# Kernel tuning notes

Measured on AMD Instinct MI355X. Metric: run time of the kernel, lower is better.

Reference implementation:

```python
import jax, jax.numpy as jnp
import numpy as np

B, N_MAX, H, STEPS = 8, 36, 64, 5


def setup_inputs() -> dict:
    key = jax.random.key(0)
    ks = jax.random.split(key, 6)
    bound = 1.0 / np.sqrt(H)
    return {
        "edge_wgt": jax.random.normal(ks[0], (B, N_MAX, N_MAX, H, H), dtype=jnp.float32) * 0.1,
        "nodes_embed": jax.random.normal(ks[1], (B, N_MAX, H), dtype=jnp.float32),
        "mask": jnp.ones((B, N_MAX, 1), dtype=jnp.float32),
        "w_ih": jax.random.uniform(ks[2], (3 * H, H), jnp.float32, -bound, bound),
        "w_hh": jax.random.uniform(ks[3], (3 * H, H), jnp.float32, -bound, bound),
        "b_ih": jax.random.uniform(ks[4], (3 * H,), jnp.float32, -bound, bound),
        "b_hh": jax.random.uniform(ks[5], (3 * H,), jnp.float32, -bound, bound),
    }


def _gru_cell(x, h, w_ih, w_hh, b_ih, b_hh):
    # torch.nn.GRUCell math; x, h: [..., H]
    gi = x @ w_ih.T + b_ih
    gh = h @ w_hh.T + b_hh
    i_r, i_z, i_n = jnp.split(gi, 3, axis=-1)
    h_r, h_z, h_n = jnp.split(gh, 3, axis=-1)
    r = jax.nn.sigmoid(i_r + h_r)
    z = jax.nn.sigmoid(i_z + h_z)
    n = jnp.tanh(i_n + r * h_n)
    return (1.0 - z) * n + z * h


def reference(edge_wgt, nodes_embed, mask, w_ih, w_hh, b_ih, b_hh):
    n_max = edge_wgt.shape[1]
    inv_n2 = 1.0 / (n_max * n_max)
    nodes = nodes_embed
    for _ in range(STEPS):
        # messages[b,j,k] = (1/n^2) * sum_{i,l} edge_wgt[b,i,j,k,l] * nodes[b,i,l]
        messages = jnp.einsum('bijkl,bil->bjk', edge_wgt, nodes) * inv_n2
        nodes = _gru_cell(messages, nodes, w_ih, w_hh, b_ih, b_hh) * mask
    return nodes
```

## Files before the change

kernel.cpp:

```cpp
#include <hip/hip_runtime.h>
#include <hip/hip_bf16.h>


#define BB 8
#define NN 36
#define HH 64
#define GG 12
#define IPG (NN / GG)
#define NSTEPS 5

__device__ __forceinline__ unsigned bf16rtn(float f) {
    unsigned u = __float_as_uint(f);
    return (u + 0x7FFFu + ((u >> 16) & 1u)) >> 16;
}

__global__ __launch_bounds__(64) void einsum_f32_cvt(
    const float* __restrict__ edge,
    const float* __restrict__ nodes,
    float* __restrict__ partial,
    uint2* __restrict__ ebf)
{
    const int lane = threadIdx.x;
    const int bid  = blockIdx.x;
    const int g = bid % GG;
    const int j = (bid / GG) % NN;
    const int b = bid / (GG * NN);

    const int l4 = lane & 15;

    float acc[16];
    #pragma unroll
    for (int it = 0; it < 16; ++it) acc[it] = 0.f;

    #pragma unroll
    for (int ii = 0; ii < IPG; ++ii) {
        const int i = g * IPG + ii;
        const float4 v = *(const float4*)(nodes + (b * NN + i) * HH + l4 * 4);
        const size_t blkElem = (size_t)((b * NN + i) * NN + j) * (HH * HH);
        const float4* __restrict__ Wb = (const float4*)(edge + blkElem);
        uint2* __restrict__ Eb = ebf + (blkElem >> 2);
        #pragma unroll
        for (int it = 0; it < 16; ++it) {
            const float4 w = Wb[it * 64 + lane];
            acc[it] = fmaf(w.x, v.x, acc[it]);
            acc[it] = fmaf(w.y, v.y, acc[it]);
            acc[it] = fmaf(w.z, v.z, acc[it]);
            acc[it] = fmaf(w.w, v.w, acc[it]);
            uint2 pk;
            pk.x = bf16rtn(w.x) | (bf16rtn(w.y) << 16);
            pk.y = bf16rtn(w.z) | (bf16rtn(w.w) << 16);
            Eb[it * 64 + lane] = pk;
        }
    }

    #pragma unroll
    for (int m = 1; m < 16; m <<= 1) {
        #pragma unroll
        for (int it = 0; it < 16; ++it)
            acc[it] += __shfl_xor(acc[it], m, 64);
    }

    const int p  = lane & 15;
    const int gq = lane >> 4;
    float outv = acc[0];
    #pragma unroll
    for (int t = 1; t < 16; ++t) outv = (p == t) ? acc[t] : outv;

    partial[(size_t)bid * HH + (4 * p + gq)] = outv;
}

__global__ __launch_bounds__(64) void einsum_bf16(
    const uint4* __restrict__ ebf,
    const float* __restrict__ nodes,
    float* __restrict__ partial)
{
    const int lane = threadIdx.x;
    const int bid  = blockIdx.x;
    const int g = bid % GG;
    const int j = (bid / GG) % NN;
    const int b = bid / (GG * NN);

    const int l8 = lane & 7;

    float acc[8];
    #pragma unroll
    for (int it = 0; it < 8; ++it) acc[it] = 0.f;

    #pragma unroll
    for (int ii = 0; ii < IPG; ++ii) {
        const int i = g * IPG + ii;
        const float* np_ = nodes + (b * NN + i) * HH + l8 * 8;
        const float4 v0 = *(const float4*)(np_);
        const float4 v1 = *(const float4*)(np_ + 4);
        const size_t blkElem = (size_t)((b * NN + i) * NN + j) * (HH * HH);
        const uint4* __restrict__ Wb = ebf + (blkElem >> 3);
        #pragma unroll
        for (int it = 0; it < 8; ++it) {
            const uint4 w = Wb[it * 64 + lane];
            acc[it] = fmaf(__uint_as_float(w.x << 16),          v0.x, acc[it]);
            acc[it] = fmaf(__uint_as_float(w.x & 0xffff0000u),  v0.y, acc[it]);
            acc[it] = fmaf(__uint_as_float(w.y << 16),          v0.z, acc[it]);
            acc[it] = fmaf(__uint_as_float(w.y & 0xffff0000u),  v0.w, acc[it]);
            acc[it] = fmaf(__uint_as_float(w.z << 16),          v1.x, acc[it]);
            acc[it] = fmaf(__uint_as_float(w.z & 0xffff0000u),  v1.y, acc[it]);
            acc[it] = fmaf(__uint_as_float(w.w << 16),          v1.z, acc[it]);
            acc[it] = fmaf(__uint_as_float(w.w & 0xffff0000u),  v1.w, acc[it]);
        }
    }

    #pragma unroll
    for (int m = 1; m < 8; m <<= 1) {
        #pragma unroll
        for (int it = 0; it < 8; ++it)
            acc[it] += __shfl_xor(acc[it], m, 64);
    }

    const int p  = lane & 7;
    const int gq = lane >> 3;
    float outv = acc[0];
    #pragma unroll
    for (int t = 1; t < 8; ++t) outv = (p == t) ? acc[t] : outv;

    partial[(size_t)bid * HH + (8 * p + gq)] = outv;
}

__global__ __launch_bounds__(64) void gru_step(
    const float* __restrict__ partial,
    const float* __restrict__ nodes_in,
    const float* __restrict__ mask,
    const float* __restrict__ w_ih,
    const float* __restrict__ w_hh,
    const float* __restrict__ b_ih,
    const float* __restrict__ b_hh,
    float* __restrict__ nodes_out)
{
    const int t  = threadIdx.x;
    const int bj = blockIdx.x;
    const float inv_n2 = 1.0f / (float)(NN * NN);

    float m = 0.f;
    #pragma unroll
    for (int g = 0; g < GG; ++g)
        m += partial[((size_t)bj * GG + g) * HH + t];
    m *= inv_n2;
    const float h = nodes_in[bj * HH + t];

    __shared__ float ms[HH];
    __shared__ float hs[HH];
    ms[t] = m;
    hs[t] = h;
    __syncthreads();

    float gi0 = b_ih[t], gi1 = b_ih[HH + t], gi2 = b_ih[2 * HH + t];
    float gh0 = b_hh[t], gh1 = b_hh[HH + t], gh2 = b_hh[2 * HH + t];

    const float4* __restrict__ wi0 = (const float4*)(w_ih + (0 * HH + t) * HH);
    const float4* __restrict__ wi1 = (const float4*)(w_ih + (1 * HH + t) * HH);
    const float4* __restrict__ wi2 = (const float4*)(w_ih + (2 * HH + t) * HH);
    const float4* __restrict__ wh0 = (const float4*)(w_hh + (0 * HH + t) * HH);
    const float4* __restrict__ wh1 = (const float4*)(w_hh + (1 * HH + t) * HH);
    const float4* __restrict__ wh2 = (const float4*)(w_hh + (2 * HH + t) * HH);

    #pragma unroll
    for (int k4 = 0; k4 < HH / 4; ++k4) {
        const float4 mv = *(const float4*)&ms[k4 * 4];
        const float4 hv = *(const float4*)&hs[k4 * 4];
        float4 a;
        a = wi0[k4]; gi0 += a.x * mv.x + a.y * mv.y + a.z * mv.z + a.w * mv.w;
        a = wi1[k4]; gi1 += a.x * mv.x + a.y * mv.y + a.z * mv.z + a.w * mv.w;
        a = wi2[k4]; gi2 += a.x * mv.x + a.y * mv.y + a.z * mv.z + a.w * mv.w;
        a = wh0[k4]; gh0 += a.x * hv.x + a.y * hv.y + a.z * hv.z + a.w * hv.w;
        a = wh1[k4]; gh1 += a.x * hv.x + a.y * hv.y + a.z * hv.z + a.w * hv.w;
        a = wh2[k4]; gh2 += a.x * hv.x + a.y * hv.y + a.z * hv.z + a.w * hv.w;
    }

    const float r = 1.f / (1.f + expf(-(gi0 + gh0)));
    const float z = 1.f / (1.f + expf(-(gi1 + gh1)));
    const float n = tanhf(gi2 + r * gh2);
    float outv = (1.f - z) * n + z * h;
    outv *= mask[bj];
    nodes_out[bj * HH + t] = outv;
}

extern "C" void kernel_launch(void* const* d_in, const int* in_sizes, int n_in,
                              void* d_out, int out_size, void* d_ws, size_t ws_size,
                              hipStream_t stream) {
    const float* edge   = (const float*)d_in[0];
    const float* nodes0 = (const float*)d_in[1];
    const float* mask   = (const float*)d_in[2];
    const float* w_ih   = (const float*)d_in[3];
    const float* w_hh   = (const float*)d_in[4];
    const float* b_ih   = (const float*)d_in[5];
    const float* b_hh   = (const float*)d_in[6];
    float* out = (float*)d_out;

    float* ws = (float*)d_ws;
    const int nodes_elems = BB * NN * HH;
    float* nodesA  = ws;
    float* nodesB  = ws + nodes_elems;
    float* partial = ws + 2 * nodes_elems;
    float* ebf_f   = partial + (size_t)BB * NN * GG * HH;
    uint2* ebf2 = (uint2*)ebf_f;
    const uint4* ebf4 = (const uint4*)ebf_f;

    const int grid_e = BB * NN * GG;

    const float* cur = nodes0;
    for (int s = 0; s < NSTEPS; ++s) {
        if (s == 0)
            einsum_f32_cvt<<<grid_e, 64, 0, stream>>>(edge, cur, partial, ebf2);
        else
            einsum_bf16<<<grid_e, 64, 0, stream>>>(ebf4, cur, partial);
        float* nxt = (s == NSTEPS - 1) ? out : ((s & 1) ? nodesB : nodesA);
        gru_step<<<BB * NN, 64, 0, stream>>>(partial, cur, mask,
                                             w_ih, w_hh, b_ih, b_hh, nxt);
        cur = nxt;
    }
}
```

Measured before the change: 151.3 us.

## Fuse GRU update into the bf16 einsum kernel with redundant per-block recompute

The separate gru_step launch is folded into the start of each following bf16 einsum kernel. Each einsum block reduces the previous step's partial sums and runs the GRU cell for its own i-nodes in shared memory, then feeds those fresh nodes into the bf16 contraction. Partial buffers are double-buffered, and a final GRU-only kernel finishes the last step. This removes four kernel launches and the global round-trip of node states. The cost is that every node's GRU is recomputed redundantly by all 36 j-blocks, which adds weight loads and serial latency at the start of each block.

```diff
diff --git a/kernel.cpp b/kernel.cpp
--- a/kernel.cpp
+++ b/kernel.cpp
@@ -8,10 +8,44 @@
 #define GG 12
 #define IPG (NN / GG)
 #define NSTEPS 5
+#define INVN2 (1.0f / (float)(NN * NN))
 
 __device__ __forceinline__ unsigned bf16rtn(float f) {
     unsigned u = __float_as_uint(f);
     return (u + 0x7FFFu + ((u >> 16) & 1u)) >> 16;
+}
+
+__device__ __forceinline__ float gru_lane(
+    const float* __restrict__ ms, const float* __restrict__ hs, int t,
+    const float* __restrict__ w_ih, const float* __restrict__ w_hh,
+    const float* __restrict__ b_ih, const float* __restrict__ b_hh)
+{
+    float gi0 = b_ih[t], gi1 = b_ih[HH + t], gi2 = b_ih[2 * HH + t];
+    float gh0 = b_hh[t], gh1 = b_hh[HH + t], gh2 = b_hh[2 * HH + t];
+
+    const float4* __restrict__ wi0 = (const float4*)(w_ih + (0 * HH + t) * HH);
+    const float4* __restrict__ wi1 = (const float4*)(w_ih + (1 * HH + t) * HH);
+    const float4* __restrict__ wi2 = (const float4*)(w_ih + (2 * HH + t) * HH);
+    const float4* __restrict__ wh0 = (const float4*)(w_hh + (0 * HH + t) * HH);
+    const float4* __restrict__ wh1 = (const float4*)(w_hh + (1 * HH + t) * HH);
+    const float4* __restrict__ wh2 = (const float4*)(w_hh + (2 * HH + t) * HH);
+
+    #pragma unroll
+    for (int k4 = 0; k4 < HH / 4; ++k4) {
+        const float4 mv = *(const float4*)&ms[k4 * 4];
+        const float4 hv = *(const float4*)&hs[k4 * 4];
+        float4 a;
+        a = wi0[k4]; gi0 += a.x * mv.x + a.y * mv.y + a.z * mv.z + a.w * mv.w;
+        a = wi1[k4]; gi1 += a.x * mv.x + a.y * mv.y + a.z * mv.z + a.w * mv.w;
+        a = wi2[k4]; gi2 += a.x * mv.x + a.y * mv.y + a.z * mv.z + a.w * mv.w;
+        a = wh0[k4]; gh0 += a.x * hv.x + a.y * hv.y + a.z * hv.z + a.w * hv.w;
+        a = wh1[k4]; gh1 += a.x * hv.x + a.y * hv.y + a.z * hv.z + a.w * hv.w;
+        a = wh2[k4]; gh2 += a.x * hv.x + a.y * hv.y + a.z * hv.z + a.w * hv.w;
+    }
+    const float r = 1.f / (1.f + expf(-(gi0 + gh0)));
+    const float z = 1.f / (1.f + expf(-(gi1 + gh1)));
+    const float n = tanhf(gi2 + r * gh2);
+    return (1.f - z) * n + z * hs[t];
 }
 
 __global__ __launch_bounds__(64) void einsum_f32_cvt(
@@ -69,16 +103,50 @@
     partial[(size_t)bid * HH + (4 * p + gq)] = outv;
 }
 
-__global__ __launch_bounds__(64) void einsum_bf16(
+__global__ __launch_bounds__(64) void einsum_bf16_fused(
     const uint4* __restrict__ ebf,
-    const float* __restrict__ nodes,
-    float* __restrict__ partial)
+    const float* __restrict__ partial_prev,
+    const float* __restrict__ nodes_pp,
+    const float* __restrict__ mask,
+    const float* __restrict__ w_ih,
+    const float* __restrict__ w_hh,
+    const float* __restrict__ b_ih,
+    const float* __restrict__ b_hh,
+    float* __restrict__ nodes_out,
+    float* __restrict__ partial_out)
 {
     const int lane = threadIdx.x;
     const int bid  = blockIdx.x;
     const int g = bid % GG;
     const int j = (bid / GG) % NN;
     const int b = bid / (GG * NN);
+    const int t = lane;
+
+    __shared__ float ms[IPG][HH];
+    __shared__ float hs[IPG][HH];
+    __shared__ float nd[IPG][HH];
+
+    #pragma unroll
+    for (int ii = 0; ii < IPG; ++ii) {
+        const int i = g * IPG + ii;
+        float m = 0.f;
+        #pragma unroll
+        for (int gp = 0; gp < GG; ++gp)
+            m += partial_prev[((size_t)(b * NN + i) * GG + gp) * HH + t];
+        ms[ii][t] = m * INVN2;
+        hs[ii][t] = nodes_pp[(b * NN + i) * HH + t];
+    }
+    __syncthreads();
+
+    #pragma unroll
+    for (int ii = 0; ii < IPG; ++ii) {
+        const int i = g * IPG + ii;
+        float outv = gru_lane(ms[ii], hs[ii], t, w_ih, w_hh, b_ih, b_hh);
+        outv *= mask[b * NN + i];
+        nd[ii][t] = outv;
+        nodes_out[(b * NN + i) * HH + t] = outv;
+    }
+    __syncthreads();
 
     const int l8 = lane & 7;
 
@@ -89,9 +157,8 @@
     #pragma unroll
     for (int ii = 0; ii < IPG; ++ii) {
         const int i = g * IPG + ii;
-        const float* np_ = nodes + (b * NN + i) * HH + l8 * 8;
-        const float4 v0 = *(const float4*)(np_);
-        const float4 v1 = *(const float4*)(np_ + 4);
+        const float4 v0 = *(const float4*)&nd[ii][l8 * 8];
+        const float4 v1 = *(const float4*)&nd[ii][l8 * 8 + 4];
         const size_t blkElem = (size_t)((b * NN + i) * NN + j) * (HH * HH);
         const uint4* __restrict__ Wb = ebf + (blkElem >> 3);
         #pragma unroll
@@ -119,12 +186,12 @@
     const int gq = lane >> 3;
     float outv = acc[0];
     #pragma unroll
-    for (int t = 1; t < 8; ++t) outv = (p == t) ? acc[t] : outv;
-
-    partial[(size_t)bid * HH + (8 * p + gq)] = outv;
-}
-
-__global__ __launch_bounds__(64) void gru_step(
+    for (int tt = 1; tt < 8; ++tt) outv = (p == tt) ? acc[tt] : outv;
+
+    partial_out[(size_t)bid * HH + (8 * p + gq)] = outv;
+}
+
+__global__ __launch_bounds__(64) void gru_final(
     const float* __restrict__ partial,
     const float* __restrict__ nodes_in,
     const float* __restrict__ mask,
@@ -136,48 +203,19 @@
 {
     const int t  = threadIdx.x;
     const int bj = blockIdx.x;
-    const float inv_n2 = 1.0f / (float)(NN * NN);
 
     float m = 0.f;
     #pragma unroll
     for (int g = 0; g < GG; ++g)
         m += partial[((size_t)bj * GG + g) * HH + t];
-    m *= inv_n2;
-    const float h = nodes_in[bj * HH + t];
 
     __shared__ float ms[HH];
     __shared__ float hs[HH];
-    ms[t] = m;
-    hs[t] = h;
+    ms[t] = m * INVN2;
+    hs[t] = nodes_in[bj * HH + t];
     __syncthreads();
 
-    float gi0 = b_ih[t], gi1 = b_ih[HH + t], gi2 = b_ih[2 * HH + t];
-    float gh0 = b_hh[t], gh1 = b_hh[HH + t], gh2 = b_hh[2 * HH + t];
-
-    const float4* __restrict__ wi0 = (const float4*)(w_ih + (0 * HH + t) * HH);
-    const float4* __restrict__ wi1 = (const float4*)(w_ih + (1 * HH + t) * HH);
-    const float4* __restrict__ wi2 = (const float4*)(w_ih + (2 * HH + t) * HH);
-    const float4* __restrict__ wh0 = (const float4*)(w_hh + (0 * HH + t) * HH);
-    const float4* __restrict__ wh1 = (const float4*)(w_hh + (1 * HH + t) * HH);
-    const float4* __restrict__ wh2 = (const float4*)(w_hh + (2 * HH + t) * HH);
-
-    #pragma unroll
-    for (int k4 = 0; k4 < HH / 4; ++k4) {
-        const float4 mv = *(const float4*)&ms[k4 * 4];
-        const float4 hv = *(const float4*)&hs[k4 * 4];
-        float4 a;
-        a = wi0[k4]; gi0 += a.x * mv.x + a.y * mv.y + a.z * mv.z + a.w * mv.w;
-        a = wi1[k4]; gi1 += a.x * mv.x + a.y * mv.y + a.z * mv.z + a.w * mv.w;
-        a = wi2[k4]; gi2 += a.x * mv.x + a.y * mv.y + a.z * mv.z + a.w * mv.w;
-        a = wh0[k4]; gh0 += a.x * hv.x + a.y * hv.y + a.z * hv.z + a.w * hv.w;
-        a = wh1[k4]; gh1 += a.x * hv.x + a.y * hv.y + a.z * hv.z + a.w * hv.w;
-        a = wh2[k4]; gh2 += a.x * hv.x + a.y * hv.y + a.z * hv.z + a.w * hv.w;
-    }
-
-    const float r = 1.f / (1.f + expf(-(gi0 + gh0)));
-    const float z = 1.f / (1.f + expf(-(gi1 + gh1)));
-    const float n = tanhf(gi2 + r * gh2);
-    float outv = (1.f - z) * n + z * h;
+    float outv = gru_lane(ms, hs, t, w_ih, w_hh, b_ih, b_hh);
     outv *= mask[bj];
     nodes_out[bj * HH + t] = outv;
 }
@@ -195,25 +233,32 @@
     float* out = (float*)d_out;
 
     float* ws = (float*)d_ws;
-    const int nodes_elems = BB * NN * HH;
-    float* nodesA  = ws;
-    float* nodesB  = ws + nodes_elems;
-    float* partial = ws + 2 * nodes_elems;
-    float* ebf_f   = partial + (size_t)BB * NN * GG * HH;
+    const int nodes_elems   = BB * NN * HH;
+    const int partial_elems = BB * NN * GG * HH;
+    float* nodesA   = ws;
+    float* nodesB   = ws + nodes_elems;
+    float* partialA = ws + 2 * nodes_elems;
+    float* partialB = partialA + partial_elems;
+    float* ebf_f    = partialB + partial_elems;
     uint2* ebf2 = (uint2*)ebf_f;
     const uint4* ebf4 = (const uint4*)ebf_f;
 
     const int grid_e = BB * NN * GG;
 
-    const float* cur = nodes0;
-    for (int s = 0; s < NSTEPS; ++s) {
-        if (s == 0)
-            einsum_f32_cvt<<<grid_e, 64, 0, stream>>>(edge, cur, partial, ebf2);
-        else
-            einsum_bf16<<<grid_e, 64, 0, stream>>>(ebf4, cur, partial);
-        float* nxt = (s == NSTEPS - 1) ? out : ((s & 1) ? nodesB : nodesA);
-        gru_step<<<BB * NN, 64, 0, stream>>>(partial, cur, mask,
-                                             w_ih, w_hh, b_ih, b_hh, nxt);
-        cur = nxt;
-    }
-}
+    einsum_f32_cvt<<<grid_e, 64, 0, stream>>>(edge, nodes0, partialA, ebf2);
+
+    einsum_bf16_fused<<<grid_e, 64, 0, stream>>>(ebf4, partialA, nodes0, mask,
+                                                 w_ih, w_hh, b_ih, b_hh,
+                                                 nodesA, partialB);
+    einsum_bf16_fused<<<grid_e, 64, 0, stream>>>(ebf4, partialB, nodesA, mask,
+                                                 w_ih, w_hh, b_ih, b_hh,
+                                                 nodesB, partialA);
+    einsum_bf16_fused<<<grid_e, 64, 0, stream>>>(ebf4, partialA, nodesB, mask,
+                                                 w_ih, w_hh, b_ih, b_hh,
+                                                 nodesA, partialB);
+    einsum_bf16_fused<<<grid_e, 64, 0, stream>>>(ebf4, partialB, nodesA, mask,
+                                                 w_ih, w_hh, b_ih, b_hh,
+                                                 nodesB, partialA);
+    gru_final<<<BB * NN, 64, 0, stream>>>(partialA, nodesB, mask,
+                                          w_ih, w_hh, b_ih, b_hh, out);
+}
```

Result: slower. 464.7 us (+207.2%).

## Fuse GRU update into einsum kernels via last-block-done atomic counters

Applied to the files above, without the earlier changes.

The separate gru_step launches are removed. Each einsum block publishes its partial sums with agent-scope stores and bumps a per-(b,j) counter, and the last of the GG blocks for that node runs the GRU tail inline. This halves the launch count and removes the inter-kernel gaps between einsum and GRU at every step. In exchange it adds a memset of the counters, atomics per block, and a serialized GRU tail on the last-arriving block.

```diff
diff --git a/kernel.cpp b/kernel.cpp
--- a/kernel.cpp
+++ b/kernel.cpp
@@ -8,23 +8,86 @@
 #define GG 12
 #define IPG (NN / GG)
 #define NSTEPS 5
+#define NBJ (BB * NN)
+#define INVN2 (1.0f / (float)(NN * NN))
 
 __device__ __forceinline__ unsigned bf16rtn(float f) {
     unsigned u = __float_as_uint(f);
     return (u + 0x7FFFu + ((u >> 16) & 1u)) >> 16;
 }
 
-__global__ __launch_bounds__(64) void einsum_f32_cvt(
+__device__ __forceinline__ float agent_load(const float* p) {
+    return __hip_atomic_load(p, __ATOMIC_RELAXED, __HIP_MEMORY_SCOPE_AGENT);
+}
+__device__ __forceinline__ void agent_store(float* p, float v) {
+    __hip_atomic_store(p, v, __ATOMIC_RELAXED, __HIP_MEMORY_SCOPE_AGENT);
+}
+
+__device__ __forceinline__ void gru_tail(
+    const float* __restrict__ partial,
+    const float* __restrict__ nodes_prev,
+    const float* __restrict__ mask,
+    const float* __restrict__ w_ih, const float* __restrict__ w_hh,
+    const float* __restrict__ b_ih, const float* __restrict__ b_hh,
+    float* __restrict__ nodes_out, int bj, int t)
+{
+    __shared__ float ms[HH];
+    __shared__ float hs[HH];
+
+    float m = 0.f;
+    #pragma unroll
+    for (int g = 0; g < GG; ++g)
+        m += agent_load(&partial[((size_t)bj * GG + g) * HH + t]);
+    ms[t] = m * INVN2;
+    hs[t] = nodes_prev[bj * HH + t];
+    __syncthreads();
+
+    float gi0 = b_ih[t], gi1 = b_ih[HH + t], gi2 = b_ih[2 * HH + t];
+    float gh0 = b_hh[t], gh1 = b_hh[HH + t], gh2 = b_hh[2 * HH + t];
+
+    const float4* __restrict__ wi0 = (const float4*)(w_ih + (0 * HH + t) * HH);
+    const float4* __restrict__ wi1 = (const float4*)(w_ih + (1 * HH + t) * HH);
+    const float4* __restrict__ wi2 = (const float4*)(w_ih + (2 * HH + t) * HH);
+    const float4* __restrict__ wh0 = (const float4*)(w_hh + (0 * HH + t) * HH);
+    const float4* __restrict__ wh1 = (const float4*)(w_hh + (1 * HH + t) * HH);
+    const float4* __restrict__ wh2 = (const float4*)(w_hh + (2 * HH + t) * HH);
+
+    #pragma unroll
+    for (int k4 = 0; k4 < HH / 4; ++k4) {
+        const float4 mv = *(const float4*)&ms[k4 * 4];
+        const float4 hv = *(const float4*)&hs[k4 * 4];
+        float4 a;
+        a = wi0[k4]; gi0 += a.x * mv.x + a.y * mv.y + a.z * mv.z + a.w * mv.w;
+        a = wi1[k4]; gi1 += a.x * mv.x + a.y * mv.y + a.z * mv.z + a.w * mv.w;
+        a = wi2[k4]; gi2 += a.x * mv.x + a.y * mv.y + a.z * mv.z + a.w * mv.w;
+        a = wh0[k4]; gh0 += a.x * hv.x + a.y * hv.y + a.z * hv.z + a.w * hv.w;
+        a = wh1[k4]; gh1 += a.x * hv.x + a.y * hv.y + a.z * hv.z + a.w * hv.w;
+        a = wh2[k4]; gh2 += a.x * hv.x + a.y * hv.y + a.z * hv.z + a.w * hv.w;
+    }
+    const float r = 1.f / (1.f + expf(-(gi0 + gh0)));
+    const float z = 1.f / (1.f + expf(-(gi1 + gh1)));
+    const float n = tanhf(gi2 + r * gh2);
+    const float outv = ((1.f - z) * n + z * hs[t]) * mask[bj];
+    nodes_out[bj * HH + t] = outv;
+}
+
+__global__ __launch_bounds__(64) void step_f32(
     const float* __restrict__ edge,
     const float* __restrict__ nodes,
+    uint2* __restrict__ ebf,
     float* __restrict__ partial,
-    uint2* __restrict__ ebf)
+    int* __restrict__ cnt,
+    const float* __restrict__ mask,
+    const float* __restrict__ w_ih, const float* __restrict__ w_hh,
+    const float* __restrict__ b_ih, const float* __restrict__ b_hh,
+    float* __restrict__ nodes_out)
 {
     const int lane = threadIdx.x;
     const int bid  = blockIdx.x;
-    const int g = bid % GG;
-    const int j = (bid / GG) % NN;
-    const int b = bid / (GG * NN);
+    const int g  = bid % GG;
+    const int bj = bid / GG;
+    const int j  = bj % NN;
+    const int b  = bj / NN;
 
     const int l4 = lane & 15;
 
@@ -66,19 +129,34 @@
     #pragma unroll
     for (int t = 1; t < 16; ++t) outv = (p == t) ? acc[t] : outv;
 
-    partial[(size_t)bid * HH + (4 * p + gq)] = outv;
-}
-
-__global__ __launch_bounds__(64) void einsum_bf16(
+    agent_store(&partial[(size_t)bid * HH + (4 * p + gq)], outv);
+
+    int old = 0;
+    if (lane == 0)
+        old = __hip_atomic_fetch_add(&cnt[bj], 1, __ATOMIC_ACQ_REL,
+                                     __HIP_MEMORY_SCOPE_AGENT);
+    old = __shfl(old, 0, 64);
+    if (old == GG - 1)
+        gru_tail(partial, nodes, mask, w_ih, w_hh, b_ih, b_hh,
+                 nodes_out, bj, lane);
+}
+
+__global__ __launch_bounds__(64) void step_bf16(
     const uint4* __restrict__ ebf,
     const float* __restrict__ nodes,
-    float* __restrict__ partial)
+    float* __restrict__ partial,
+    int* __restrict__ cnt,
+    const float* __restrict__ mask,
+    const float* __restrict__ w_ih, const float* __restrict__ w_hh,
+    const float* __restrict__ b_ih, const float* __restrict__ b_hh,
+    float* __restrict__ nodes_out)
 {
     const int lane = threadIdx.x;
     const int bid  = blockIdx.x;
-    const int g = bid % GG;
-    const int j = (bid / GG) % NN;
-    const int b = bid / (GG * NN);
+    const int g  = bid % GG;
+    const int bj = bid / GG;
+    const int j  = bj % NN;
+    const int b  = bj / NN;
 
     const int l8 = lane & 7;
 
@@ -119,67 +197,18 @@
     const int gq = lane >> 3;
     float outv = acc[0];
     #pragma unroll
-    for (int t = 1; t < 8; ++t) outv = (p == t) ? acc[t] : outv;
-
-    partial[(size_t)bid * HH + (8 * p + gq)] = outv;
-}
-
-__global__ __launch_bounds__(64) void gru_step(
-    const float* __restrict__ partial,
-    const float* __restrict__ nodes_in,
-    const float* __restrict__ mask,
-    const float* __restrict__ w_ih,
-    const float* __restrict__ w_hh,
-    const float* __restrict__ b_ih,
-    const float* __restrict__ b_hh,
-    float* __restrict__ nodes_out)
-{
-    const int t  = threadIdx.x;
-    const int bj = blockIdx.x;
-    const float inv_n2 = 1.0f / (float)(NN * NN);
-
-    float m = 0.f;
-    #pragma unroll
-    for (int g = 0; g < GG; ++g)
-        m += partial[((size_t)bj * GG + g) * HH + t];
-    m *= inv_n2;
-    const float h = nodes_in[bj * HH + t];
-
-    __shared__ float ms[HH];
-    __shared__ float hs[HH];
-    ms[t] = m;
-    hs[t] = h;
-    __syncthreads();
-
-    float gi0 = b_ih[t], gi1 = b_ih[HH + t], gi2 = b_ih[2 * HH + t];
-    float gh0 = b_hh[t], gh1 = b_hh[HH + t], gh2 = b_hh[2 * HH + t];
-
-    const float4* __restrict__ wi0 = (const float4*)(w_ih + (0 * HH + t) * HH);
-    const float4* __restrict__ wi1 = (const float4*)(w_ih + (1 * HH + t) * HH);
-    const float4* __restrict__ wi2 = (const float4*)(w_ih + (2 * HH + t) * HH);
-    const float4* __restrict__ wh0 = (const float4*)(w_hh + (0 * HH + t) * HH);
-    const float4* __restrict__ wh1 = (const float4*)(w_hh + (1 * HH + t) * HH);
-    const float4* __restrict__ wh2 = (const float4*)(w_hh + (2 * HH + t) * HH);
-
-    #pragma unroll
-    for (int k4 = 0; k4 < HH / 4; ++k4) {
-        const float4 mv = *(const float4*)&ms[k4 * 4];
-        const float4 hv = *(const float4*)&hs[k4 * 4];
-        float4 a;
-        a = wi0[k4]; gi0 += a.x * mv.x + a.y * mv.y + a.z * mv.z + a.w * mv.w;
-        a = wi1[k4]; gi1 += a.x * mv.x + a.y * mv.y + a.z * mv.z + a.w * mv.w;
-        a = wi2[k4]; gi2 += a.x * mv.x + a.y * mv.y + a.z * mv.z + a.w * mv.w;
-        a = wh0[k4]; gh0 += a.x * hv.x + a.y * hv.y + a.z * hv.z + a.w * hv.w;
-        a = wh1[k4]; gh1 += a.x * hv.x + a.y * hv.y + a.z * hv.z + a.w * hv.w;
-        a = wh2[k4]; gh2 += a.x * hv.x + a.y * hv.y + a.z * hv.z + a.w * hv.w;
-    }
-
-    const float r = 1.f / (1.f + expf(-(gi0 + gh0)));
-    const float z = 1.f / (1.f + expf(-(gi1 + gh1)));
-    const float n = tanhf(gi2 + r * gh2);
-    float outv = (1.f - z) * n + z * h;
-    outv *= mask[bj];
-    nodes_out[bj * HH + t] = outv;
+    for (int tt = 1; tt < 8; ++tt) outv = (p == tt) ? acc[tt] : outv;
+
+    agent_store(&partial[(size_t)bid * HH + (8 * p + gq)], outv);
+
+    int old = 0;
+    if (lane == 0)
+        old = __hip_atomic_fetch_add(&cnt[bj], 1, __ATOMIC_ACQ_REL,
+                                     __HIP_MEMORY_SCOPE_AGENT);
+    old = __shfl(old, 0, 64);
+    if (old == GG - 1)
+        gru_tail(partial, nodes, mask, w_ih, w_hh, b_ih, b_hh,
+                 nodes_out, bj, lane);
 }
 
 extern "C" void kernel_launch(void* const* d_in, const int* in_sizes, int n_in,
@@ -195,25 +224,33 @@
     float* out = (float*)d_out;
 
     float* ws = (float*)d_ws;
-    const int nodes_elems = BB * NN * HH;
+    const int nodes_elems   = BB * NN * HH;
+    const int partial_elems = NBJ * GG * HH;
     float* nodesA  = ws;
     float* nodesB  = ws + nodes_elems;
     float* partial = ws + 2 * nodes_elems;
-    float* ebf_f   = partial + (size_t)BB * NN * GG * HH;
+    int*   cnt     = (int*)(partial + partial_elems);
+    float* ebf_f   = (float*)(cnt + NSTEPS * NBJ);
     uint2* ebf2 = (uint2*)ebf_f;
     const uint4* ebf4 = (const uint4*)ebf_f;
 
-    const int grid_e = BB * NN * GG;
-
-    const float* cur = nodes0;
-    for (int s = 0; s < NSTEPS; ++s) {
-        if (s == 0)
-            einsum_f32_cvt<<<grid_e, 64, 0, stream>>>(edge, cur, partial, ebf2);
-        else
-            einsum_bf16<<<grid_e, 64, 0, stream>>>(ebf4, cur, partial);
-        float* nxt = (s == NSTEPS - 1) ? out : ((s & 1) ? nodesB : nodesA);
-        gru_step<<<BB * NN, 64, 0, stream>>>(partial, cur, mask,
-                                             w_ih, w_hh, b_ih, b_hh, nxt);
-        cur = nxt;
-    }
-}
+    const int grid_e = NBJ * GG;
+
+    hipMemsetAsync(cnt, 0, NSTEPS * NBJ * sizeof(int), stream);
+
+    step_f32<<<grid_e, 64, 0, stream>>>(edge, nodes0, ebf2, partial,
+                                        cnt + 0 * NBJ, mask,
+                                        w_ih, w_hh, b_ih, b_hh, nodesA);
+    step_bf16<<<grid_e, 64, 0, stream>>>(ebf4, nodesA, partial,
+                                         cnt + 1 * NBJ, mask,
+                                         w_ih, w_hh, b_ih, b_hh, nodesB);
+    step_bf16<<<grid_e, 64, 0, stream>>>(ebf4, nodesB, partial,
+                                         cnt + 2 * NBJ, mask,
+                                         w_ih, w_hh, b_ih, b_hh, nodesA);
+    step_bf16<<<grid_e, 64, 0, stream>>>(ebf4, nodesA, partial,
+                                         cnt + 3 * NBJ, mask,
+                                         w_ih, w_hh, b_ih, b_hh, nodesB);
+    step_bf16<<<grid_e, 64, 0, stream>>>(ebf4, nodesB, partial,
+                                         cnt + 4 * NBJ, mask,
+                                         w_ih, w_hh, b_ih, b_hh, out);
+}
```

Measured after the change: 570.5 us. 277% more time.
